# Kernel tuning notes

Measured on AMD Instinct MI355X. Metric: run time of the kernel, lower is better.

Reference implementation:

```python
import jax, jax.numpy as jnp
import numpy as np

DIM = 512
HEADS = 4
DIM_HEAD = 128


def setup_inputs() -> dict:
    key = jax.random.key(0)
    k_x, k_w, k_b = jax.random.split(key, 3)
    x = jax.random.normal(k_x, (2, 4096, DIM), dtype=jnp.float32)
    # nn.Linear(dim, 3*heads*dim_head): weight [out, in], torch init ~ U(-1/sqrt(in), 1/sqrt(in))
    bound = 1.0 / np.sqrt(DIM)
    W = jax.random.uniform(k_w, (3 * HEADS * DIM_HEAD, DIM), minval=-bound, maxval=bound, dtype=jnp.float32)
    b = jax.random.uniform(k_b, (3 * HEADS * DIM_HEAD,), minval=-bound, maxval=bound, dtype=jnp.float32)
    return {"x": x, "W": W, "b": b}


def _split_heads(t):
    # rearrange 'b r (d h) -> b h r d' with h=HEADS: heads is the INNER factor
    bsz, n, _ = t.shape
    t = t.reshape(bsz, n, DIM_HEAD, HEADS)  # [b, n, d, h]
    return jnp.transpose(t, (0, 3, 1, 2))    # [b, h, n, d]


def reference(x, W, b):
    scale = DIM_HEAD ** -0.5
    qkv = jnp.einsum('bnd,od->bno', x, W) + b          # [b, n, 3*h*dh]
    q, k, v = jnp.split(qkv, 3, axis=2)
    q = _split_heads(q) * scale                         # [b, h, n, dh]
    k = _split_heads(k)
    v = _split_heads(v)
    sim = jnp.einsum('bhld,bhkd->bhlk', q, k)           # [b, h, n, n]
    attn = jax.nn.softmax(sim, axis=-1)
    out = jnp.einsum('bhqk,bhkd->bhqd', attn, v)        # [b, h, n, dh]
    # rearrange 'b h l d -> b l (h d)'
    bsz, h, n, dh = out.shape
    return jnp.transpose(out, (0, 2, 1, 3)).reshape(bsz, n, h * dh)
```

## Files before the change

kernel.cpp:

```cpp
#include <hip/hip_runtime.h>
#include <math.h>
#include <stdint.h>

#define SEQ 4096
#define DMODEL 512
#define NH 4
#define DH 128

typedef short s16x8 __attribute__((ext_vector_type(8)));
typedef float f32x4 __attribute__((ext_vector_type(4)));

__device__ __forceinline__ ushort f2bf(float f) {
    uint32_t u = __builtin_bit_cast(uint32_t, f);
    u += 0x7FFFu + ((u >> 16) & 1u);
    return (ushort)(u >> 16);
}

__device__ __forceinline__ void gl2lds16(const void* g, void* l) {
    __builtin_amdgcn_global_load_lds(
        (const __attribute__((address_space(1))) uint32_t*)g,
        (__attribute__((address_space(3))) uint32_t*)l, 16, 0, 0);
}

__global__ __launch_bounds__(256) void cast_bf16(
    const float* __restrict__ src, ushort* __restrict__ dst)
{
    const size_t i = ((size_t)blockIdx.x * 256 + threadIdx.x) * 8;
    float4 f0 = *(const float4*)&src[i];
    float4 f1 = *(const float4*)&src[i + 4];
    s16x8 o;
    o[0] = (short)f2bf(f0.x); o[1] = (short)f2bf(f0.y);
    o[2] = (short)f2bf(f0.z); o[3] = (short)f2bf(f0.w);
    o[4] = (short)f2bf(f1.x); o[5] = (short)f2bf(f1.y);
    o[6] = (short)f2bf(f1.z); o[7] = (short)f2bf(f1.w);
    *(s16x8*)&dst[i] = o;
}

__global__ __launch_bounds__(256) void qkv_gemm(
    const ushort* __restrict__ xb, const ushort* __restrict__ Wb,
    const float* __restrict__ bias,
    ushort* __restrict__ Qb, ushort* __restrict__ Kb, ushort* __restrict__ Vt)
{
    __shared__ char As[16384];
    __shared__ char Bs[16384];

    const int t   = threadIdx.x;
    const int l   = t & 63;
    const int w   = t >> 6;
    const int l15 = l & 15;
    const int g   = l >> 4;
    const int n0  = blockIdx.x * 128;
    const int m0  = blockIdx.y * 128;
    const int wr  = w >> 1, wc = w & 1;

    f32x4 acc[4][4];
#pragma unroll
    for (int mi = 0; mi < 4; ++mi)
#pragma unroll
        for (int ni = 0; ni < 4; ++ni) acc[mi][ni] = (f32x4)(0.f);

    for (int step = 0; step < 8; ++step) {
        const int k0 = step * 64;
        __syncthreads();
#pragma unroll
        for (int it = 0; it < 4; ++it) {
            const int slot = it * 256 + t;
            const int r    = slot >> 3;
            const int cs   = slot & 7;
            const int c    = cs ^ (r & 7);
            char* lA = As + (size_t)(it * 256 + 64 * w) * 16;
            gl2lds16(xb + (size_t)(m0 + r) * DMODEL + k0 + c * 8, lA);
            char* lB = Bs + (size_t)(it * 256 + 64 * w) * 16;
            gl2lds16(Wb + (size_t)(n0 + r) * DMODEL + k0 + c * 8, lB);
        }
        __syncthreads();

#pragma unroll
        for (int ks = 0; ks < 2; ++ks) {
            s16x8 af[4], bf[4];
#pragma unroll
            for (int mi = 0; mi < 4; ++mi) {
                const int row = 64 * wr + 16 * mi + l15;
                const int ch  = (4 * ks + g) ^ (row & 7);
                af[mi] = *(const s16x8*)(As + row * 128 + ch * 16);
            }
#pragma unroll
            for (int ni = 0; ni < 4; ++ni) {
                const int row = 64 * wc + 16 * ni + l15;
                const int ch  = (4 * ks + g) ^ (row & 7);
                bf[ni] = *(const s16x8*)(Bs + row * 128 + ch * 16);
            }
#pragma unroll
            for (int mi = 0; mi < 4; ++mi)
#pragma unroll
                for (int ni = 0; ni < 4; ++ni)
                    acc[mi][ni] = __builtin_amdgcn_mfma_f32_16x16x32_bf16(
                        af[mi], bf[ni], acc[mi][ni], 0, 0, 0);
        }
    }

    const float scale = 0.08838834764831845f;
#pragma unroll
    for (int ni = 0; ni < 4; ++ni) {
        const int o     = n0 + 64 * wc + 16 * ni + l15;
        const float bv  = bias[o];
        const int which = o >> 9;
        const int rem   = o & 511;
        const int d     = rem >> 2;
        const int h     = rem & 3;
#pragma unroll
        for (int mi = 0; mi < 4; ++mi)
#pragma unroll
            for (int i = 0; i < 4; ++i) {
                const int m    = m0 + 64 * wr + 16 * mi + 4 * g + i;
                const int bidx = m >> 12;
                const int npos = m & 4095;
                const int bhh  = bidx * NH + h;
                const float val = acc[mi][ni][i] + bv;
                if (which == 0)
                    Qb[((size_t)bhh * SEQ + npos) * DH + d] = f2bf(val * scale);
                else if (which == 1)
                    Kb[((size_t)bhh * SEQ + npos) * DH + d] = f2bf(val);
                else
                    Vt[((size_t)bhh * DH + d) * SEQ + npos] = f2bf(val);
            }
    }
}

__global__ __launch_bounds__(256) void flash_attn_mfma(
    const ushort* __restrict__ Qb, const ushort* __restrict__ Kb,
    const ushort* __restrict__ Vt, float* __restrict__ out)
{
    extern __shared__ char smem[];
    char* KsB = smem;
    char* VsB = smem + 32768;
    char* PsB = smem + 65536;

    const int t   = threadIdx.x;
    const int l   = t & 63;
    const int w   = t >> 6;
    const int l15 = l & 15;
    const int g   = l >> 4;
    const int q0  = blockIdx.x * 128;
    const int bh  = blockIdx.y;
    const int b   = bh >> 2, h = bh & 3;

    s16x8 qf[2][4];
    {
        const ushort* qbase = Qb + ((size_t)bh * SEQ + q0 + 32 * w) * DH;
#pragma unroll
        for (int m = 0; m < 2; ++m)
#pragma unroll
            for (int ks = 0; ks < 4; ++ks)
                qf[m][ks] = *(const s16x8*)&qbase[(size_t)(16 * m + l15) * DH + 32 * ks + 8 * g];
    }

    f32x4 O[2][8];
    f32x4 Ol[2];
#pragma unroll
    for (int m = 0; m < 2; ++m) {
        Ol[m] = (f32x4)(0.f);
#pragma unroll
        for (int db = 0; db < 8; ++db) O[m][db] = (f32x4)(0.f);
    }

    s16x8 onesf;
    {
        const short o = (l15 == 0) ? (short)0x3F80 : (short)0;
#pragma unroll
        for (int j = 0; j < 8; ++j) onesf[j] = o;
    }

    const size_t kgbase = (size_t)bh * SEQ * DH;
    const size_t vgbase = (size_t)bh * DH * SEQ;
    char* Pw = PsB + w * 8192;

    for (int kt = 0; kt < SEQ / 128; ++kt) {
        __syncthreads();
#pragma unroll
        for (int it = 0; it < 8; ++it) {
            const int slot = it * 256 + t;
            const int r    = slot >> 4;
            const int cs   = slot & 15;
            const int c    = cs ^ (r & 15);
            char* lK = KsB + (size_t)(it * 256 + 64 * w) * 16;
            gl2lds16(Kb + kgbase + (size_t)(kt * 128 + r) * DH + c * 8, lK);
            char* lV = VsB + (size_t)(it * 256 + 64 * w) * 16;
            gl2lds16(Vt + vgbase + (size_t)r * SEQ + kt * 128 + c * 8, lV);
        }
        __syncthreads();

        f32x4 sAcc[2][8];
#pragma unroll
        for (int m = 0; m < 2; ++m)
#pragma unroll
            for (int nb = 0; nb < 8; ++nb) sAcc[m][nb] = (f32x4)(0.f);

#pragma unroll
        for (int ks = 0; ks < 4; ++ks) {
#pragma unroll
            for (int nb = 0; nb < 8; ++nb) {
                const int n  = 16 * nb + l15;
                const int ch = (ks * 4 + g) ^ l15;
                s16x8 kf = *(const s16x8*)(KsB + n * 256 + ch * 16);
                sAcc[0][nb] = __builtin_amdgcn_mfma_f32_16x16x32_bf16(qf[0][ks], kf, sAcc[0][nb], 0, 0, 0);
                sAcc[1][nb] = __builtin_amdgcn_mfma_f32_16x16x32_bf16(qf[1][ks], kf, sAcc[1][nb], 0, 0, 0);
            }
        }

#pragma unroll
        for (int m = 0; m < 2; ++m)
#pragma unroll
            for (int nb = 0; nb < 8; ++nb)
#pragma unroll
                for (int i = 0; i < 4; ++i) {
                    const float p  = __expf(sAcc[m][nb][i]);
                    const int row  = 16 * m + 4 * g + i;
                    const int col  = 16 * nb + l15;
                    const int e    = row * 128 + (col ^ ((row & 7) << 3));
                    *(ushort*)(Pw + e * 2) = f2bf(p);
                }

#pragma unroll
        for (int ks = 0; ks < 4; ++ks) {
            s16x8 pa[2];
#pragma unroll
            for (int m = 0; m < 2; ++m) {
                const int row = 16 * m + l15;
                const int e   = row * 128 + ((ks * 32 + 8 * g) ^ ((row & 7) << 3));
                pa[m] = *(const s16x8*)(Pw + e * 2);
            }
            Ol[0] = __builtin_amdgcn_mfma_f32_16x16x32_bf16(pa[0], onesf, Ol[0], 0, 0, 0);
            Ol[1] = __builtin_amdgcn_mfma_f32_16x16x32_bf16(pa[1], onesf, Ol[1], 0, 0, 0);
#pragma unroll
            for (int db = 0; db < 8; ++db) {
                const int d  = 16 * db + l15;
                const int ch = (ks * 4 + g) ^ l15;
                s16x8 vf = *(const s16x8*)(VsB + d * 256 + ch * 16);
                O[0][db] = __builtin_amdgcn_mfma_f32_16x16x32_bf16(pa[0], vf, O[0][db], 0, 0, 0);
                O[1][db] = __builtin_amdgcn_mfma_f32_16x16x32_bf16(pa[1], vf, O[1][db], 0, 0, 0);
            }
        }
    }

#pragma unroll
    for (int m = 0; m < 2; ++m)
#pragma unroll
        for (int i = 0; i < 4; ++i) {
            const float lsum = __shfl(Ol[m][i], l & 48);
            const float inv  = 1.f / lsum;
            const int q = q0 + 32 * w + 16 * m + 4 * g + i;
            float* dst = out + ((size_t)b * SEQ + q) * DMODEL + h * DH;
#pragma unroll
            for (int db = 0; db < 8; ++db)
                dst[16 * db + l15] = O[m][db][i] * inv;
        }
}

extern "C" void kernel_launch(void* const* d_in, const int* in_sizes, int n_in,
                              void* d_out, int out_size, void* d_ws, size_t ws_size,
                              hipStream_t stream) {
    const float* x    = (const float*)d_in[0];
    const float* W    = (const float*)d_in[1];
    const float* bias = (const float*)d_in[2];
    float* outp = (float*)d_out;

    ushort* xb = (ushort*)d_ws;
    ushort* Wb = xb + (size_t)2 * SEQ * DMODEL;
    ushort* Qb = Wb + (size_t)3 * NH * DH * DMODEL;
    ushort* Kb = Qb + (size_t)2 * NH * SEQ * DH;
    ushort* Vt = Kb + (size_t)2 * NH * SEQ * DH;

    hipFuncSetAttribute((const void*)flash_attn_mfma,
                        hipFuncAttributeMaxDynamicSharedMemorySize, 98304);

    cast_bf16<<<2048, 256, 0, stream>>>(x, xb);
    cast_bf16<<<384, 256, 0, stream>>>(W, Wb);
    qkv_gemm<<<dim3(12, 64), 256, 0, stream>>>(xb, Wb, bias, Qb, Kb, Vt);
    flash_attn_mfma<<<dim3(32, 8), 256, 98304, stream>>>(Qb, Kb, Vt, outp);
}
```

Measured before the change: 260.5 us.

## Split attention KV range in two and merge partials in a combine kernel

The flash attention kernel now runs 512-thread blocks covering 256 queries each, and each block handles only half of the key/value sequence. Each split writes unnormalized partial outputs and row sums to workspace, and a new combine kernel adds the two halves, normalizes, and writes the interleaved output. The aim is more resident waves per block for latency hiding, more reuse of each staged K/V tile across queries, and a shorter serial loop per block. The cost is extra global traffic for the fp32 partials, one more kernel launch, and larger LDS use per block.

```diff
diff --git a/kernel.cpp b/kernel.cpp
--- a/kernel.cpp
+++ b/kernel.cpp
@@ -127,23 +127,25 @@
     }
 }
 
-__global__ __launch_bounds__(256) void flash_attn_mfma(
+__global__ __launch_bounds__(512) void flash_attn_mfma(
     const ushort* __restrict__ Qb, const ushort* __restrict__ Kb,
-    const ushort* __restrict__ Vt, float* __restrict__ out)
+    const ushort* __restrict__ Vt,
+    float* __restrict__ Opart, float* __restrict__ lpart)
 {
     extern __shared__ char smem[];
     char* KsB = smem;
     char* VsB = smem + 32768;
     char* PsB = smem + 65536;
 
-    const int t   = threadIdx.x;
-    const int l   = t & 63;
-    const int w   = t >> 6;
-    const int l15 = l & 15;
-    const int g   = l >> 4;
-    const int q0  = blockIdx.x * 128;
-    const int bh  = blockIdx.y;
-    const int b   = bh >> 2, h = bh & 3;
+    const int t     = threadIdx.x;
+    const int l     = t & 63;
+    const int w     = t >> 6;
+    const int l15   = l & 15;
+    const int g     = l >> 4;
+    const int xs    = blockIdx.x;
+    const int bh    = xs >> 1;
+    const int split = xs & 1;
+    const int q0    = blockIdx.y * 256;
 
     s16x8 qf[2][4];
     {
@@ -175,17 +177,18 @@
     const size_t vgbase = (size_t)bh * DH * SEQ;
     char* Pw = PsB + w * 8192;
 
-    for (int kt = 0; kt < SEQ / 128; ++kt) {
+    const int kt0 = split * 16;
+    for (int kt = kt0; kt < kt0 + 16; ++kt) {
         __syncthreads();
 #pragma unroll
-        for (int it = 0; it < 8; ++it) {
-            const int slot = it * 256 + t;
+        for (int it = 0; it < 4; ++it) {
+            const int slot = it * 512 + t;
             const int r    = slot >> 4;
             const int cs   = slot & 15;
             const int c    = cs ^ (r & 15);
-            char* lK = KsB + (size_t)(it * 256 + 64 * w) * 16;
+            char* lK = KsB + (size_t)(it * 512 + 64 * w) * 16;
             gl2lds16(Kb + kgbase + (size_t)(kt * 128 + r) * DH + c * 8, lK);
-            char* lV = VsB + (size_t)(it * 256 + 64 * w) * 16;
+            char* lV = VsB + (size_t)(it * 512 + 64 * w) * 16;
             gl2lds16(Vt + vgbase + (size_t)r * SEQ + kt * 128 + c * 8, lV);
         }
         __syncthreads();
@@ -243,18 +246,56 @@
         }
     }
 
+    float* obase = Opart + ((size_t)(split * 8 + bh) * SEQ + q0 + 32 * w) * DH;
 #pragma unroll
     for (int m = 0; m < 2; ++m)
 #pragma unroll
         for (int i = 0; i < 4; ++i) {
-            const float lsum = __shfl(Ol[m][i], l & 48);
-            const float inv  = 1.f / lsum;
-            const int q = q0 + 32 * w + 16 * m + 4 * g + i;
-            float* dst = out + ((size_t)b * SEQ + q) * DMODEL + h * DH;
+            const int r = 16 * m + 4 * g + i;
+            float* dst = obase + (size_t)r * DH;
 #pragma unroll
             for (int db = 0; db < 8; ++db)
-                dst[16 * db + l15] = O[m][db][i] * inv;
-        }
+                dst[16 * db + l15] = O[m][db][i];
+        }
+    if (l15 == 0) {
+        float* lbase = lpart + (size_t)(split * 8 + bh) * SEQ + q0 + 32 * w;
+#pragma unroll
+        for (int m = 0; m < 2; ++m)
+#pragma unroll
+            for (int i = 0; i < 4; ++i)
+                lbase[16 * m + 4 * g + i] = Ol[m][i];
+    }
+}
+
+__global__ __launch_bounds__(256) void attn_combine(
+    const float* __restrict__ Opart, const float* __restrict__ lpart,
+    float* __restrict__ out)
+{
+    const int f = blockIdx.x * 256 + threadIdx.x;
+    const int c = f & 63;
+    const int n = (f >> 6) & 4095;
+    const int b = f >> 18;
+    const int h = c >> 4;
+    const int d = (c & 15) * 8;
+    const int bh = b * NH + h;
+
+    const size_t o0 = ((size_t)bh * SEQ + n) * DH + d;
+    const size_t o1 = ((size_t)(8 + bh) * SEQ + n) * DH + d;
+    float4 a0 = *(const float4*)&Opart[o0];
+    float4 a1 = *(const float4*)&Opart[o0 + 4];
+    float4 b0 = *(const float4*)&Opart[o1];
+    float4 b1 = *(const float4*)&Opart[o1 + 4];
+    const float inv = 1.f / (lpart[(size_t)bh * SEQ + n] + lpart[(size_t)(8 + bh) * SEQ + n]);
+
+    float4 r0, r1;
+    r0.x = (a0.x + b0.x) * inv; r0.y = (a0.y + b0.y) * inv;
+    r0.z = (a0.z + b0.z) * inv; r0.w = (a0.w + b0.w) * inv;
+    r1.x = (a1.x + b1.x) * inv; r1.y = (a1.y + b1.y) * inv;
+    r1.z = (a1.z + b1.z) * inv; r1.w = (a1.w + b1.w) * inv;
+
+    float* dst = out + ((size_t)b * SEQ + n) * DMODEL + h * DH + d;
+    *(float4*)&dst[0] = r0;
+    *(float4*)&dst[4] = r1;
 }
 
 extern "C" void kernel_launch(void* const* d_in, const int* in_sizes, int n_in,
@@ -270,12 +311,15 @@
     ushort* Qb = Wb + (size_t)3 * NH * DH * DMODEL;
     ushort* Kb = Qb + (size_t)2 * NH * SEQ * DH;
     ushort* Vt = Kb + (size_t)2 * NH * SEQ * DH;
+    float* Opart = (float*)(Vt + (size_t)2 * NH * SEQ * DH);
+    float* lpart = Opart + (size_t)2 * 2 * NH * SEQ * DH;
 
     hipFuncSetAttribute((const void*)flash_attn_mfma,
-                        hipFuncAttributeMaxDynamicSharedMemorySize, 98304);
+                        hipFuncAttributeMaxDynamicSharedMemorySize, 131072);
 
     cast_bf16<<<2048, 256, 0, stream>>>(x, xb);
     cast_bf16<<<384, 256, 0, stream>>>(W, Wb);
     qkv_gemm<<<dim3(12, 64), 256, 0, stream>>>(xb, Wb, bias, Qb, Kb, Vt);
-    flash_attn_mfma<<<dim3(32, 8), 256, 98304, stream>>>(Qb, Kb, Vt, outp);
-}
+    flash_attn_mfma<<<dim3(16, 16), 512, 131072, stream>>>(Qb, Kb, Vt, Opart, lpart);
+    attn_combine<<<2048, 256, 0, stream>>>(Opart, lpart, outp);
+}
```

Result: faster. 246.5 us (-5.4%).
